# Performance work log

Measured on AMD Instinct MI355X. Metric: run time of the kernel, lower is better.

Reference implementation:

```python
import jax, jax.numpy as jnp
import numpy as np

# RReLU in eval mode acts as leaky-relu with slope (lower+upper)/2, defaults 1/8, 1/3
RRELU_SLOPE = (1.0 / 8.0 + 1.0 / 3.0) / 2.0

T, N, F, H, C, O, E = 8, 50000, 128, 128, 64, 2, 800000
HM1 = H - 1  # second GCN layer / MLP input width = hidden_feat - 1


def _glorot(k, shape):
    a = np.sqrt(6.0 / (shape[-2] + shape[-1])).astype(np.float32)
    return jax.random.uniform(k, shape, jnp.float32, -a, a)


def setup_inputs() -> dict:
    key = jax.random.key(0)
    ks = jax.random.split(key, 16)
    inp = {}
    inp["feats"] = jax.random.normal(ks[0], (T, N, F), jnp.float32)
    inp["src"] = jax.random.randint(ks[1], (E,), 0, N, jnp.int32)
    inp["dst"] = jax.random.randint(ks[2], (E,), 0, N, jnp.int32)
    # initial GCN weights (xavier_uniform as in reset_parameters)
    inp["W1_0"] = _glorot(ks[3], (F, H))
    inp["W2_0"] = _glorot(ks[4], (H, HM1))
    # mat-GRU cell 1 (rows=F, cols=H): gates stacked [z, r, h]
    inp["g1_W"] = jax.random.normal(ks[5], (3, F, F), jnp.float32) * 0.05
    inp["g1_U"] = jax.random.normal(ks[6], (3, F, F), jnp.float32) * 0.05
    inp["g1_b"] = jnp.zeros((3, F, H), jnp.float32)
    # mat-GRU cell 2 (rows=H, cols=H-1)
    inp["g2_W"] = jax.random.normal(ks[7], (3, H, H), jnp.float32) * 0.05
    inp["g2_U"] = jax.random.normal(ks[8], (3, H, H), jnp.float32) * 0.05
    inp["g2_b"] = jnp.zeros((3, H, HM1), jnp.float32)
    # MLP head
    inp["mlp_w1"] = _glorot(ks[9], (HM1, C))
    inp["mlp_b1"] = jnp.zeros((C,), jnp.float32)
    inp["mlp_w2"] = _glorot(ks[10], (C, O))
    inp["mlp_b2"] = jnp.zeros((O,), jnp.float32)
    return inp


def _mat_gru(gW, gU, gb, Wh):
    # EvolveGCN-O: weight matrix is both input and hidden of the GRU
    z = jax.nn.sigmoid(gW[0] @ Wh + gU[0] @ Wh + gb[0])
    r = jax.nn.sigmoid(gW[1] @ Wh + gU[1] @ Wh + gb[1])
    h_til = jnp.tanh(gW[2] @ Wh + gU[2] @ (r * Wh) + gb[2])
    return (1.0 - z) * Wh + z * h_til


def reference(feats, W1_0, W2_0, g1_W, g1_U, g1_b, g2_W, g2_U, g2_b,
              mlp_w1, mlp_b1, mlp_w2, mlp_b2, src, dst):
    n = feats.shape[1]
    ones = jnp.ones(src.shape, jnp.float32)
    deg_out = jax.ops.segment_sum(ones, src, num_segments=n)
    deg_in = jax.ops.segment_sum(ones, dst, num_segments=n)
    # symmetric GCN normalization D_out^-1/2 A D_in^-1/2 on edge list
    norm = (jax.lax.rsqrt(jnp.maximum(deg_out, 1.0))[src]
            * jax.lax.rsqrt(jnp.maximum(deg_in, 1.0))[dst])  # [E]

    def aggregate(x):  # x: [N, d] -> [N, d]
        return jax.ops.segment_sum(x[src] * norm[:, None], dst, num_segments=n)

    def step(carry, x):
        W1, W2, _ = carry
        W1 = _mat_gru(g1_W, g1_U, g1_b, W1)
        W2 = _mat_gru(g2_W, g2_U, g2_b, W2)
        h1 = aggregate(x @ W1)                      # [N, H]
        h1 = jnp.where(h1 >= 0, h1, RRELU_SLOPE * h1)  # RReLU (eval-mode)
        h2 = aggregate(h1 @ W2)                     # [N, H-1]
        return (W1, W2, h2), None

    feat0 = jnp.zeros((n, W2_0.shape[1]), feats.dtype)
    (W1, W2, feat_end), _ = jax.lax.scan(step, (W1_0, W2_0, feat0), feats)
    out = jnp.maximum(feat_end @ mlp_w1 + mlp_b1, 0.0) @ mlp_w2 + mlp_b2
    return out
```

## Files before the change

kernel.cpp:

```cpp
#include <hip/hip_runtime.h>


#define HM1 127

static constexpr float RRELU_SLOPE = (1.0f / 8.0f + 1.0f / 3.0f) * 0.5f;

__device__ __forceinline__ float sigmoidf_(float x) {
    return 1.0f / (1.0f + expf(-x));
}

__global__ __launch_bounds__(256) void phase1(
    const int* __restrict__ src, const int* __restrict__ dst,
    int* __restrict__ degO, int* __restrict__ degI, int E, int nbE,
    const float* __restrict__ g1W, const float* __restrict__ g1U,
    const float* __restrict__ g2W, const float* __restrict__ g2U,
    float* __restrict__ AT)
{
    int bid = blockIdx.x;
    if (bid < nbE) {
        int e = bid * 256 + threadIdx.x;
        if (e < E) {
            atomicAdd(&degO[src[e]], 1);
            atomicAdd(&degI[dst[e]], 1);
        }
    } else {
        int t = (bid - nbE) * 256 + threadIdx.x;
        int m = t >> 14;
        int k = (t >> 7) & 127;
        int i = t & 127;
        const float* W = (m < 4) ? g1W : g2W;
        const float* U = (m < 4) ? g1U : g2U;
        int which = m & 3;
        float v;
        if (which == 0)      v = W[i * 128 + k] + U[i * 128 + k];
        else if (which == 1) v = W[16384 + i * 128 + k] + U[16384 + i * 128 + k];
        else if (which == 2) v = W[32768 + i * 128 + k];
        else                 v = U[32768 + i * 128 + k];
        AT[t] = v;
    }
}

__global__ __launch_bounds__(256) void phase2(
    const float* __restrict__ W1_0, const float* __restrict__ W2_0,
    const float* __restrict__ AT,
    const float* __restrict__ g1b, const float* __restrict__ g2b,
    float* __restrict__ W1f, float* __restrict__ W2f,
    const int* __restrict__ degO, const int* __restrict__ degI,
    float* __restrict__ rdegO, float* __restrict__ rdegI,
    int* __restrict__ row_ptr, int N)
{
    __shared__ float smem[512];
    int bid = blockIdx.x;
    if (bid < 128) {
        const int half = threadIdx.x >> 7;
        const int i = threadIdx.x & 127;
        int c = bid * 2 + half;
        if (c > 254) c = 254;
        const int cell = (c >= 128) ? 1 : 0;
        const int cc = cell ? (c - 128) : c;

        const float* A  = AT + cell * 4 * 16384;
        const float* A0 = A;
        const float* A1 = A + 16384;
        const float* B0 = A + 32768;
        const float* B1 = A + 49152;
        const float* gb = cell ? g2b : g1b;
        const int   ldb = cell ? HM1 : 128;
        const float* W0 = cell ? W2_0 : W1_0;
        const int   ldw = cell ? HM1 : 128;

        float* w  = smem + half * 128;
        float* rw = smem + 256 + half * 128;

        const float zb = gb[i * ldb + cc];
        const float rb = gb[128 * ldb + i * ldb + cc];
        const float hb = gb[2 * 128 * ldb + i * ldb + cc];
        float wi = W0[i * ldw + cc];
        w[i] = wi;
        __syncthreads();

        for (int s = 0; s < 8; ++s) {
            float zacc = zb, racc = rb, tacc = hb;
            #pragma unroll 4
            for (int k = 0; k < 128; ++k) {
                float wk = w[k];
                zacc += A0[k * 128 + i] * wk;
                racc += A1[k * 128 + i] * wk;
                tacc += B0[k * 128 + i] * wk;
            }
            float r = sigmoidf_(racc);
            rw[i] = r * wi;
            __syncthreads();
            #pragma unroll 4
            for (int k = 0; k < 128; ++k)
                tacc += B1[k * 128 + i] * rw[k];
            float z = sigmoidf_(zacc);
            float t = tanhf(tacc);
            float nwi = (1.0f - z) * wi + z * t;
            __syncthreads();
            wi = nwi;
            w[i] = nwi;
            __syncthreads();
        }
        float* Wf = cell ? W2f : W1f;
        Wf[i * 128 + cc] = wi;
    } else if (bid == 128) {
        int* sums = (int*)smem;
        const int t = threadIdx.x;
        const int chunk = (N + 255) / 256;
        const int lo = t * chunk;
        const int hi = min(lo + chunk, N);
        int s = 0;
        for (int i2 = lo; i2 < hi; ++i2) s += degI[i2];
        sums[t] = s;
        __syncthreads();
        for (int off = 1; off < 256; off <<= 1) {
            int v = (t >= off) ? sums[t - off] : 0;
            __syncthreads();
            sums[t] += v;
            __syncthreads();
        }
        int base = (t > 0) ? sums[t - 1] : 0;
        for (int i2 = lo; i2 < hi; ++i2) {
            row_ptr[i2] = base;
            base += degI[i2];
        }
        if (t == 255) row_ptr[N] = sums[255];
    } else {
        int n = (bid - 129) * 256 + threadIdx.x;
        if (n < N) {
            rdegO[n] = rsqrtf(fmaxf((float)degO[n], 1.0f));
            rdegI[n] = rsqrtf(fmaxf((float)degI[n], 1.0f));
        }
    }
}

__global__ __launch_bounds__(256) void phase3(
    const int* __restrict__ src, const int* __restrict__ dst,
    const int* __restrict__ row_ptr, int* __restrict__ cursor,
    int* __restrict__ srcs, int E, int nbE,
    const float* __restrict__ x7, const float* __restrict__ W1f,
    const float* __restrict__ rdegO, float* __restrict__ Zs, int N, int nbN,
    const float* __restrict__ W2f, const float* __restrict__ mw1,
    float* __restrict__ W2m)
{
    int bid = blockIdx.x;
    if (bid < nbE) {
        int e = bid * 256 + threadIdx.x;
        if (e < E) {
            int d = dst[e];
            int pos = row_ptr[d] + atomicAdd(&cursor[d], 1);
            srcs[pos] = src[e];
        }
    } else if (bid < nbE + 2 * nbN) {
        int b = bid - nbE;
        int half = b & 1;
        int row = (b >> 1) * 256 + threadIdx.x;
        int c0 = half * 64;
        if (row >= N) return;

        float acc[64];
        #pragma unroll
        for (int j = 0; j < 64; ++j) acc[j] = 0.0f;

        const float4* xr = reinterpret_cast<const float4*>(x7 + (size_t)row * 128);
        for (int k4 = 0; k4 < 32; ++k4) {
            float4 xv = xr[k4];
            const float* wr = W1f + (k4 * 4) * 128 + c0;
            #pragma unroll
            for (int j = 0; j < 64; ++j) acc[j] += xv.x * wr[j];
            wr += 128;
            #pragma unroll
            for (int j = 0; j < 64; ++j) acc[j] += xv.y * wr[j];
            wr += 128;
            #pragma unroll
            for (int j = 0; j < 64; ++j) acc[j] += xv.z * wr[j];
            wr += 128;
            #pragma unroll
            for (int j = 0; j < 64; ++j) acc[j] += xv.w * wr[j];
        }

        float ro = rdegO[row];
        float* zr = Zs + (size_t)row * 128 + c0;
        #pragma unroll
        for (int j = 0; j < 64; j += 4) {
            float4 v;
            v.x = acc[j] * ro; v.y = acc[j + 1] * ro;
            v.z = acc[j + 2] * ro; v.w = acc[j + 3] * ro;
            *reinterpret_cast<float4*>(zr + j) = v;
        }
    } else {
        int idx = (bid - nbE - 2 * nbN) * 256 + threadIdx.x;
        int i = idx >> 6, j = idx & 63;
        float acc = 0.0f;
        for (int k = 0; k < HM1; ++k)
            acc += W2f[i * 128 + k] * mw1[k * 64 + j];
        W2m[idx] = acc;
    }
}

__global__ __launch_bounds__(256) void gather128(
    const float* __restrict__ Zs, const int* __restrict__ srcs,
    const int* __restrict__ row_ptr, const float* __restrict__ rdegI,
    float* __restrict__ H1, int N)
{
    int n = (blockIdx.x * 256 + threadIdx.x) >> 6;
    int lane = threadIdx.x & 63;
    if (n >= N) return;
    int lo = row_ptr[n], hi = row_ptr[n + 1];
    float ax = 0.0f, ay = 0.0f;
    for (int base = lo; base < hi; base += 64) {
        int cnt = min(hi - base, 64);
        int idx = (lane < cnt) ? srcs[base + lane] : 0;
        int j = 0;
        for (; j + 8 <= cnt; j += 8) {
            int s0 = __shfl(idx, j + 0), s1 = __shfl(idx, j + 1);
            int s2 = __shfl(idx, j + 2), s3 = __shfl(idx, j + 3);
            int s4 = __shfl(idx, j + 4), s5 = __shfl(idx, j + 5);
            int s6 = __shfl(idx, j + 6), s7 = __shfl(idx, j + 7);
            float2 v0 = *reinterpret_cast<const float2*>(Zs + (size_t)s0 * 128 + lane * 2);
            float2 v1 = *reinterpret_cast<const float2*>(Zs + (size_t)s1 * 128 + lane * 2);
            float2 v2 = *reinterpret_cast<const float2*>(Zs + (size_t)s2 * 128 + lane * 2);
            float2 v3 = *reinterpret_cast<const float2*>(Zs + (size_t)s3 * 128 + lane * 2);
            float2 v4 = *reinterpret_cast<const float2*>(Zs + (size_t)s4 * 128 + lane * 2);
            float2 v5 = *reinterpret_cast<const float2*>(Zs + (size_t)s5 * 128 + lane * 2);
            float2 v6 = *reinterpret_cast<const float2*>(Zs + (size_t)s6 * 128 + lane * 2);
            float2 v7 = *reinterpret_cast<const float2*>(Zs + (size_t)s7 * 128 + lane * 2);
            ax += v0.x + v1.x + v2.x + v3.x + v4.x + v5.x + v6.x + v7.x;
            ay += v0.y + v1.y + v2.y + v3.y + v4.y + v5.y + v6.y + v7.y;
        }
        for (; j < cnt; ++j) {
            int s0 = __shfl(idx, j);
            float2 v0 = *reinterpret_cast<const float2*>(Zs + (size_t)s0 * 128 + lane * 2);
            ax += v0.x;
            ay += v0.y;
        }
    }
    float ri = rdegI[n];
    ax *= ri; ay *= ri;
    ax = ax >= 0.0f ? ax : RRELU_SLOPE * ax;
    ay = ay >= 0.0f ? ay : RRELU_SLOPE * ay;
    float2 o; o.x = ax; o.y = ay;
    *reinterpret_cast<float2*>(H1 + (size_t)n * 128 + lane * 2) = o;
}

__global__ __launch_bounds__(256) void gemm_y(
    const float* __restrict__ H1, const float* __restrict__ W2m,
    const float* __restrict__ rdegO, float* __restrict__ Ys, int N)
{
    int row = blockIdx.x * 256 + threadIdx.x;
    if (row >= N) return;

    float acc[64];
    #pragma unroll
    for (int j = 0; j < 64; ++j) acc[j] = 0.0f;

    const float4* hr = reinterpret_cast<const float4*>(H1 + (size_t)row * 128);
    for (int k4 = 0; k4 < 32; ++k4) {
        float4 h = hr[k4];
        const float* wr = W2m + (k4 * 4) * 64;
        #pragma unroll
        for (int j = 0; j < 64; ++j) acc[j] += h.x * wr[j];
        wr += 64;
        #pragma unroll
        for (int j = 0; j < 64; ++j) acc[j] += h.y * wr[j];
        wr += 64;
        #pragma unroll
        for (int j = 0; j < 64; ++j) acc[j] += h.z * wr[j];
        wr += 64;
        #pragma unroll
        for (int j = 0; j < 64; ++j) acc[j] += h.w * wr[j];
    }

    float ro = rdegO[row];
    float* yr = Ys + (size_t)row * 64;
    #pragma unroll
    for (int j = 0; j < 64; j += 4) {
        float4 v;
        v.x = acc[j] * ro; v.y = acc[j + 1] * ro;
        v.z = acc[j + 2] * ro; v.w = acc[j + 3] * ro;
        *reinterpret_cast<float4*>(yr + j) = v;
    }
}

__global__ __launch_bounds__(256) void gather64_mlp(
    const float* __restrict__ Ys, const int* __restrict__ srcs,
    const int* __restrict__ row_ptr, const float* __restrict__ rdegI,
    const float* __restrict__ b1, const float* __restrict__ w2,
    const float* __restrict__ b2, float* __restrict__ out, int N)
{
    int n = (blockIdx.x * 256 + threadIdx.x) >> 6;
    int lane = threadIdx.x & 63;
    if (n >= N) return;
    int lo = row_ptr[n], hi = row_ptr[n + 1];
    float acc = 0.0f;
    for (int base = lo; base < hi; base += 64) {
        int cnt = min(hi - base, 64);
        int idx = (lane < cnt) ? srcs[base + lane] : 0;
        int j = 0;
        for (; j + 8 <= cnt; j += 8) {
            int s0 = __shfl(idx, j + 0), s1 = __shfl(idx, j + 1);
            int s2 = __shfl(idx, j + 2), s3 = __shfl(idx, j + 3);
            int s4 = __shfl(idx, j + 4), s5 = __shfl(idx, j + 5);
            int s6 = __shfl(idx, j + 6), s7 = __shfl(idx, j + 7);
            acc += Ys[(size_t)s0 * 64 + lane] + Ys[(size_t)s1 * 64 + lane]
                 + Ys[(size_t)s2 * 64 + lane] + Ys[(size_t)s3 * 64 + lane]
                 + Ys[(size_t)s4 * 64 + lane] + Ys[(size_t)s5 * 64 + lane]
                 + Ys[(size_t)s6 * 64 + lane] + Ys[(size_t)s7 * 64 + lane];
        }
        for (; j < cnt; ++j) {
            int s0 = __shfl(idx, j);
            acc += Ys[(size_t)s0 * 64 + lane];
        }
    }
    float z = acc * rdegI[n];
    float t = fmaxf(z + b1[lane], 0.0f);
    float p0 = t * w2[lane * 2 + 0];
    float p1 = t * w2[lane * 2 + 1];
    #pragma unroll
    for (int off = 32; off; off >>= 1) {
        p0 += __shfl_xor(p0, off);
        p1 += __shfl_xor(p1, off);
    }
    if (lane == 0) {
        out[(size_t)n * 2 + 0] = p0 + b2[0];
        out[(size_t)n * 2 + 1] = p1 + b2[1];
    }
}

extern "C" void kernel_launch(void* const* d_in, const int* in_sizes, int n_in,
                              void* d_out, int out_size, void* d_ws, size_t ws_size,
                              hipStream_t stream) {
    const float* feats = (const float*)d_in[0];
    const int*   src   = (const int*)d_in[1];
    const int*   dst   = (const int*)d_in[2];
    const float* W1_0  = (const float*)d_in[3];
    const float* W2_0  = (const float*)d_in[4];
    const float* g1W   = (const float*)d_in[5];
    const float* g1U   = (const float*)d_in[6];
    const float* g1b   = (const float*)d_in[7];
    const float* g2W   = (const float*)d_in[8];
    const float* g2U   = (const float*)d_in[9];
    const float* g2b   = (const float*)d_in[10];
    const float* mw1   = (const float*)d_in[11];
    const float* mb1   = (const float*)d_in[12];
    const float* mw2   = (const float*)d_in[13];
    const float* mb2   = (const float*)d_in[14];
    float* out = (float*)d_out;

    const int E = in_sizes[1];
    const int N = in_sizes[0] / (8 * 128);
    const int nbE = (E + 255) / 256;
    const int nbN = (N + 255) / 256;

    float* ws    = (float*)d_ws;
    float* W1f   = ws;
    float* W2f   = W1f + 16384;
    float* W2m   = W2f + 16384;
    float* AT    = W2m + 8192;
    float* rdegO = AT + 8 * 16384;
    float* rdegI = rdegO + N;
    int*   degO  = (int*)(rdegI + N);
    int*   degI  = degO + N;
    int*   cursor= degI + N;
    int*   row_ptr = cursor + N;
    int*   srcs  = row_ptr + N + 1;
    float* Zs    = (float*)(srcs + E);
    float* H1    = Zs + (size_t)N * 128;
    float* Ys    = Zs;

    const float* x7 = feats + (size_t)7 * N * 128;

    hipMemsetAsync(degO, 0, sizeof(int) * 3 * (size_t)N, stream);

    phase1<<<nbE + 512, 256, 0, stream>>>(src, dst, degO, degI, E, nbE,
                                          g1W, g1U, g2W, g2U, AT);

    phase2<<<129 + nbN, 256, 0, stream>>>(W1_0, W2_0, AT, g1b, g2b, W1f, W2f,
                                          degO, degI, rdegO, rdegI, row_ptr, N);

    phase3<<<nbE + 2 * nbN + 32, 256, 0, stream>>>(
        src, dst, row_ptr, cursor, srcs, E, nbE,
        x7, W1f, rdegO, Zs, N, nbN, W2f, mw1, W2m);

    int ngather = ((N * 64) + 255) / 256;
    gather128<<<ngather, 256, 0, stream>>>(Zs, srcs, row_ptr, rdegI, H1, N);

    gemm_y<<<nbN, 256, 0, stream>>>(H1, W2m, rdegO, Ys, N);

    gather64_mlp<<<ngather, 256, 0, stream>>>(Ys, srcs, row_ptr, rdegI,
                                              mb1, mw2, mb2, out, N);
}
```

Measured before the change: 635.7 us.

## Fuse gather with second GEMM, retile first GEMM, parallelize scan and transpose

Several changes land together. The gather128 and gemm_y kernels merge into one phase4 kernel that aggregates each node's row into shared memory and immediately multiplies it by W2m, so the H1 intermediate never goes through global memory. The x@W1 GEMM is retiled so each thread computes 4 rows by 16 columns with float4 weight loads, replacing one row by 64 columns per thread, which should improve weight reuse and register pressure. The single-block prefix scan now uses wave shuffles instead of serial per-thread chunks, and the GRU weight transpose moves into 32 shared-memory tiled blocks for coalesced access; in exchange the scan still runs in one block and the fused kernel adds a block barrier.

```diff
diff --git a/kernel.cpp b/kernel.cpp
--- a/kernel.cpp
+++ b/kernel.cpp
@@ -11,32 +11,49 @@
 
 __global__ __launch_bounds__(256) void phase1(
     const int* __restrict__ src, const int* __restrict__ dst,
-    int* __restrict__ degO, int* __restrict__ degI, int E, int nbE,
+    int* __restrict__ degO, int* __restrict__ degI, int E,
     const float* __restrict__ g1W, const float* __restrict__ g1U,
     const float* __restrict__ g2W, const float* __restrict__ g2U,
     float* __restrict__ AT)
 {
     int bid = blockIdx.x;
-    if (bid < nbE) {
-        int e = bid * 256 + threadIdx.x;
+    if (bid < 32) {
+        __shared__ float tile[64][65];
+        int m     = bid >> 2;
+        int itile = bid & 1;
+        int ktile = (bid >> 1) & 1;
+        const float* W = (m < 4) ? g1W : g2W;
+        const float* U = (m < 4) ? g1U : g2U;
+        int which = m & 3;
+        const float* P;
+        const float* Q2 = nullptr;
+        if (which == 0)      { P = W;         Q2 = U; }
+        else if (which == 1) { P = W + 16384; Q2 = U + 16384; }
+        else if (which == 2) { P = W + 32768; }
+        else                 { P = U + 32768; }
+        int c  = threadIdx.x & 63;
+        int r4 = threadIdx.x >> 6;
+        #pragma unroll
+        for (int rr = 0; rr < 16; ++rr) {
+            int row = itile * 64 + rr * 4 + r4;
+            int col = ktile * 64 + c;
+            float v = P[row * 128 + col];
+            if (Q2) v += Q2[row * 128 + col];
+            tile[rr * 4 + r4][c] = v;
+        }
+        __syncthreads();
+        float* ATm = AT + m * 16384;
+        #pragma unroll
+        for (int rr = 0; rr < 16; ++rr) {
+            int krow = ktile * 64 + rr * 4 + r4;
+            ATm[krow * 128 + itile * 64 + c] = tile[c][rr * 4 + r4];
+        }
+    } else {
+        int e = (bid - 32) * 256 + threadIdx.x;
         if (e < E) {
             atomicAdd(&degO[src[e]], 1);
             atomicAdd(&degI[dst[e]], 1);
         }
-    } else {
-        int t = (bid - nbE) * 256 + threadIdx.x;
-        int m = t >> 14;
-        int k = (t >> 7) & 127;
-        int i = t & 127;
-        const float* W = (m < 4) ? g1W : g2W;
-        const float* U = (m < 4) ? g1U : g2U;
-        int which = m & 3;
-        float v;
-        if (which == 0)      v = W[i * 128 + k] + U[i * 128 + k];
-        else if (which == 1) v = W[16384 + i * 128 + k] + U[16384 + i * 128 + k];
-        else if (which == 2) v = W[32768 + i * 128 + k];
-        else                 v = U[32768 + i * 128 + k];
-        AT[t] = v;
     }
 }
 
@@ -105,27 +122,33 @@
         float* Wf = cell ? W2f : W1f;
         Wf[i * 128 + cc] = wi;
     } else if (bid == 128) {
-        int* sums = (int*)smem;
-        const int t = threadIdx.x;
-        const int chunk = (N + 255) / 256;
-        const int lo = t * chunk;
-        const int hi = min(lo + chunk, N);
+        __shared__ int qsum[4];
+        const int t = threadIdx.x, w = t >> 6, l = t & 63;
+        const int Q = (((N + 3) >> 2) + 63) & ~63;
+        const int qlo = w * Q;
+        const int qhi = min(qlo + Q, N);
         int s = 0;
-        for (int i2 = lo; i2 < hi; ++i2) s += degI[i2];
-        sums[t] = s;
+        for (int i2 = qlo + l; i2 < qhi; i2 += 64) s += degI[i2];
+        #pragma unroll
+        for (int d = 32; d; d >>= 1) s += __shfl_xor(s, d);
+        if (l == 0) qsum[w] = s;
         __syncthreads();
-        for (int off = 1; off < 256; off <<= 1) {
-            int v = (t >= off) ? sums[t - off] : 0;
-            __syncthreads();
-            sums[t] += v;
-            __syncthreads();
-        }
-        int base = (t > 0) ? sums[t - 1] : 0;
-        for (int i2 = lo; i2 < hi; ++i2) {
-            row_ptr[i2] = base;
-            base += degI[i2];
-        }
-        if (t == 255) row_ptr[N] = sums[255];
+        int base = 0;
+        for (int q = 0; q < w; ++q) base += qsum[q];
+        if (t == 0) row_ptr[N] = qsum[0] + qsum[1] + qsum[2] + qsum[3];
+        int carry = base;
+        for (int b = qlo; b < qhi; b += 64) {
+            int i2 = b + l;
+            int v = (i2 < qhi) ? degI[i2] : 0;
+            int incl = v;
+            #pragma unroll
+            for (int d = 1; d < 64; d <<= 1) {
+                int nbr = __shfl_up(incl, d);
+                if (l >= d) incl += nbr;
+            }
+            if (i2 < qhi) row_ptr[i2] = carry + incl - v;
+            carry += __shfl(incl, 63);
+        }
     } else {
         int n = (bid - 129) * 256 + threadIdx.x;
         if (n < N) {
@@ -140,7 +163,7 @@
     const int* __restrict__ row_ptr, int* __restrict__ cursor,
     int* __restrict__ srcs, int E, int nbE,
     const float* __restrict__ x7, const float* __restrict__ W1f,
-    const float* __restrict__ rdegO, float* __restrict__ Zs, int N, int nbN,
+    const float* __restrict__ rdegO, float* __restrict__ Zs, int N, int ngz,
     const float* __restrict__ W2f, const float* __restrict__ mw1,
     float* __restrict__ W2m)
 {
@@ -152,45 +175,67 @@
             int pos = row_ptr[d] + atomicAdd(&cursor[d], 1);
             srcs[pos] = src[e];
         }
-    } else if (bid < nbE + 2 * nbN) {
-        int b = bid - nbE;
-        int half = b & 1;
-        int row = (b >> 1) * 256 + threadIdx.x;
-        int c0 = half * 64;
-        if (row >= N) return;
-
-        float acc[64];
+    } else if (bid < nbE + ngz) {
+        int b  = bid - nbE;
+        int cb = b & 7;
+        int rg = b >> 3;
+        int c0 = cb * 16;
+        int r0 = rg * 1024 + threadIdx.x;
+
+        float acc[4][16];
         #pragma unroll
-        for (int j = 0; j < 64; ++j) acc[j] = 0.0f;
-
-        const float4* xr = reinterpret_cast<const float4*>(x7 + (size_t)row * 128);
+        for (int r = 0; r < 4; ++r)
+            #pragma unroll
+            for (int j = 0; j < 16; ++j) acc[r][j] = 0.0f;
+
+        const float4* x0p = (const float4*)(x7 + (size_t)min(r0,       N - 1) * 128);
+        const float4* x1p = (const float4*)(x7 + (size_t)min(r0 + 256, N - 1) * 128);
+        const float4* x2p = (const float4*)(x7 + (size_t)min(r0 + 512, N - 1) * 128);
+        const float4* x3p = (const float4*)(x7 + (size_t)min(r0 + 768, N - 1) * 128);
+
         for (int k4 = 0; k4 < 32; ++k4) {
-            float4 xv = xr[k4];
-            const float* wr = W1f + (k4 * 4) * 128 + c0;
-            #pragma unroll
-            for (int j = 0; j < 64; ++j) acc[j] += xv.x * wr[j];
-            wr += 128;
-            #pragma unroll
-            for (int j = 0; j < 64; ++j) acc[j] += xv.y * wr[j];
-            wr += 128;
-            #pragma unroll
-            for (int j = 0; j < 64; ++j) acc[j] += xv.z * wr[j];
-            wr += 128;
-            #pragma unroll
-            for (int j = 0; j < 64; ++j) acc[j] += xv.w * wr[j];
-        }
-
-        float ro = rdegO[row];
-        float* zr = Zs + (size_t)row * 128 + c0;
+            float4 v0 = x0p[k4], v1 = x1p[k4], v2 = x2p[k4], v3 = x3p[k4];
+            const float* wb = W1f + (k4 * 4) * 128 + c0;
+#define ZSTEP(KK, S0, S1, S2, S3)                                           \
+            {                                                               \
+                const float* wr_ = wb + (KK) * 128;                         \
+                float4 wa = *(const float4*)(wr_ + 0);                      \
+                float4 wq = *(const float4*)(wr_ + 4);                      \
+                float4 wc = *(const float4*)(wr_ + 8);                      \
+                float4 wd = *(const float4*)(wr_ + 12);                     \
+                float w16[16] = {wa.x, wa.y, wa.z, wa.w, wq.x, wq.y, wq.z, wq.w, \
+                                 wc.x, wc.y, wc.z, wc.w, wd.x, wd.y, wd.z, wd.w}; \
+                float ss[4] = {S0, S1, S2, S3};                             \
+                _Pragma("unroll")                                           \
+                for (int r = 0; r < 4; ++r) {                               \
+                    _Pragma("unroll")                                       \
+                    for (int j = 0; j < 16; ++j) acc[r][j] += ss[r] * w16[j]; \
+                }                                                           \
+            }
+            ZSTEP(0, v0.x, v1.x, v2.x, v3.x)
+            ZSTEP(1, v0.y, v1.y, v2.y, v3.y)
+            ZSTEP(2, v0.z, v1.z, v2.z, v3.z)
+            ZSTEP(3, v0.w, v1.w, v2.w, v3.w)
+#undef ZSTEP
+        }
+
         #pragma unroll
-        for (int j = 0; j < 64; j += 4) {
-            float4 v;
-            v.x = acc[j] * ro; v.y = acc[j + 1] * ro;
-            v.z = acc[j + 2] * ro; v.w = acc[j + 3] * ro;
-            *reinterpret_cast<float4*>(zr + j) = v;
+        for (int r = 0; r < 4; ++r) {
+            int row = r0 + r * 256;
+            if (row < N) {
+                float ro = rdegO[row];
+                float* zr = Zs + (size_t)row * 128 + c0;
+                #pragma unroll
+                for (int j = 0; j < 16; j += 4) {
+                    float4 o;
+                    o.x = acc[r][j] * ro;     o.y = acc[r][j + 1] * ro;
+                    o.z = acc[r][j + 2] * ro; o.w = acc[r][j + 3] * ro;
+                    *(float4*)(zr + j) = o;
+                }
+            }
         }
     } else {
-        int idx = (bid - nbE - 2 * nbN) * 256 + threadIdx.x;
+        int idx = (bid - nbE - ngz) * 256 + threadIdx.x;
         int i = idx >> 6, j = idx & 63;
         float acc = 0.0f;
         for (int k = 0; k < HM1; ++k)
@@ -199,91 +244,63 @@
     }
 }
 
-__global__ __launch_bounds__(256) void gather128(
+__global__ __launch_bounds__(256) void phase4(
     const float* __restrict__ Zs, const int* __restrict__ srcs,
     const int* __restrict__ row_ptr, const float* __restrict__ rdegI,
-    float* __restrict__ H1, int N)
+    const float* __restrict__ rdegO, const float* __restrict__ W2m,
+    float* __restrict__ Ys, int N)
 {
-    int n = (blockIdx.x * 256 + threadIdx.x) >> 6;
-    int lane = threadIdx.x & 63;
-    if (n >= N) return;
-    int lo = row_ptr[n], hi = row_ptr[n + 1];
+    __shared__ float h[4][128];
+    const int t = threadIdx.x, w = t >> 6, l = t & 63;
+    const int n = blockIdx.x * 4 + w;
+    int lo = 0, hi = 0;
+    float ri = 0.0f;
+    if (n < N) { lo = row_ptr[n]; hi = row_ptr[n + 1]; ri = rdegI[n]; }
     float ax = 0.0f, ay = 0.0f;
     for (int base = lo; base < hi; base += 64) {
         int cnt = min(hi - base, 64);
-        int idx = (lane < cnt) ? srcs[base + lane] : 0;
+        int idx = (l < cnt) ? srcs[base + l] : 0;
         int j = 0;
         for (; j + 8 <= cnt; j += 8) {
             int s0 = __shfl(idx, j + 0), s1 = __shfl(idx, j + 1);
             int s2 = __shfl(idx, j + 2), s3 = __shfl(idx, j + 3);
             int s4 = __shfl(idx, j + 4), s5 = __shfl(idx, j + 5);
             int s6 = __shfl(idx, j + 6), s7 = __shfl(idx, j + 7);
-            float2 v0 = *reinterpret_cast<const float2*>(Zs + (size_t)s0 * 128 + lane * 2);
-            float2 v1 = *reinterpret_cast<const float2*>(Zs + (size_t)s1 * 128 + lane * 2);
-            float2 v2 = *reinterpret_cast<const float2*>(Zs + (size_t)s2 * 128 + lane * 2);
-            float2 v3 = *reinterpret_cast<const float2*>(Zs + (size_t)s3 * 128 + lane * 2);
-            float2 v4 = *reinterpret_cast<const float2*>(Zs + (size_t)s4 * 128 + lane * 2);
-            float2 v5 = *reinterpret_cast<const float2*>(Zs + (size_t)s5 * 128 + lane * 2);
-            float2 v6 = *reinterpret_cast<const float2*>(Zs + (size_t)s6 * 128 + lane * 2);
-            float2 v7 = *reinterpret_cast<const float2*>(Zs + (size_t)s7 * 128 + lane * 2);
+            float2 v0 = *(const float2*)(Zs + (size_t)s0 * 128 + l * 2);
+            float2 v1 = *(const float2*)(Zs + (size_t)s1 * 128 + l * 2);
+            float2 v2 = *(const float2*)(Zs + (size_t)s2 * 128 + l * 2);
+            float2 v3 = *(const float2*)(Zs + (size_t)s3 * 128 + l * 2);
+            float2 v4 = *(const float2*)(Zs + (size_t)s4 * 128 + l * 2);
+            float2 v5 = *(const float2*)(Zs + (size_t)s5 * 128 + l * 2);
+            float2 v6 = *(const float2*)(Zs + (size_t)s6 * 128 + l * 2);
+            float2 v7 = *(const float2*)(Zs + (size_t)s7 * 128 + l * 2);
             ax += v0.x + v1.x + v2.x + v3.x + v4.x + v5.x + v6.x + v7.x;
             ay += v0.y + v1.y + v2.y + v3.y + v4.y + v5.y + v6.y + v7.y;
         }
         for (; j < cnt; ++j) {
             int s0 = __shfl(idx, j);
-            float2 v0 = *reinterpret_cast<const float2*>(Zs + (size_t)s0 * 128 + lane * 2);
+            float2 v0 = *(const float2*)(Zs + (size_t)s0 * 128 + l * 2);
             ax += v0.x;
             ay += v0.y;
         }
     }
-    float ri = rdegI[n];
     ax *= ri; ay *= ri;
     ax = ax >= 0.0f ? ax : RRELU_SLOPE * ax;
     ay = ay >= 0.0f ? ay : RRELU_SLOPE * ay;
-    float2 o; o.x = ax; o.y = ay;
-    *reinterpret_cast<float2*>(H1 + (size_t)n * 128 + lane * 2) = o;
-}
-
-__global__ __launch_bounds__(256) void gemm_y(
-    const float* __restrict__ H1, const float* __restrict__ W2m,
-    const float* __restrict__ rdegO, float* __restrict__ Ys, int N)
-{
-    int row = blockIdx.x * 256 + threadIdx.x;
-    if (row >= N) return;
-
-    float acc[64];
-    #pragma unroll
-    for (int j = 0; j < 64; ++j) acc[j] = 0.0f;
-
-    const float4* hr = reinterpret_cast<const float4*>(H1 + (size_t)row * 128);
-    for (int k4 = 0; k4 < 32; ++k4) {
-        float4 h = hr[k4];
-        const float* wr = W2m + (k4 * 4) * 64;
-        #pragma unroll
-        for (int j = 0; j < 64; ++j) acc[j] += h.x * wr[j];
-        wr += 64;
-        #pragma unroll
-        for (int j = 0; j < 64; ++j) acc[j] += h.y * wr[j];
-        wr += 64;
-        #pragma unroll
-        for (int j = 0; j < 64; ++j) acc[j] += h.z * wr[j];
-        wr += 64;
-        #pragma unroll
-        for (int j = 0; j < 64; ++j) acc[j] += h.w * wr[j];
-    }
-
-    float ro = rdegO[row];
-    float* yr = Ys + (size_t)row * 64;
-    #pragma unroll
-    for (int j = 0; j < 64; j += 4) {
-        float4 v;
-        v.x = acc[j] * ro; v.y = acc[j + 1] * ro;
-        v.z = acc[j + 2] * ro; v.w = acc[j + 3] * ro;
-        *reinterpret_cast<float4*>(yr + j) = v;
-    }
-}
-
-__global__ __launch_bounds__(256) void gather64_mlp(
+    *(float2*)&h[w][2 * l] = make_float2(ax, ay);
+    __syncthreads();
+
+    const int n2 = blockIdx.x * 4 + w;
+    if (n2 < N) {
+        const float* hr = h[w];
+        float a = 0.0f;
+        #pragma unroll 8
+        for (int k = 0; k < 128; ++k) a += hr[k] * W2m[k * 64 + l];
+        Ys[(size_t)n2 * 64 + l] = a * rdegO[n2];
+    }
+}
+
+__global__ __launch_bounds__(256) void phase5(
     const float* __restrict__ Ys, const int* __restrict__ srcs,
     const int* __restrict__ row_ptr, const float* __restrict__ rdegI,
     const float* __restrict__ b1, const float* __restrict__ w2,
@@ -352,6 +369,7 @@
     const int N = in_sizes[0] / (8 * 128);
     const int nbE = (E + 255) / 256;
     const int nbN = (N + 255) / 256;
+    const int ngz = ((N + 1023) / 1024) * 8;
 
     float* ws    = (float*)d_ws;
     float* W1f   = ws;
@@ -366,28 +384,25 @@
     int*   row_ptr = cursor + N;
     int*   srcs  = row_ptr + N + 1;
     float* Zs    = (float*)(srcs + E);
-    float* H1    = Zs + (size_t)N * 128;
-    float* Ys    = Zs;
+    float* Ys    = Zs + (size_t)N * 128;
 
     const float* x7 = feats + (size_t)7 * N * 128;
 
     hipMemsetAsync(degO, 0, sizeof(int) * 3 * (size_t)N, stream);
 
-    phase1<<<nbE + 512, 256, 0, stream>>>(src, dst, degO, degI, E, nbE,
-                                          g1W, g1U, g2W, g2U, AT);
+    phase1<<<32 + nbE, 256, 0, stream>>>(src, dst, degO, degI, E,
+                                         g1W, g1U, g2W, g2U, AT);
 
     phase2<<<129 + nbN, 256, 0, stream>>>(W1_0, W2_0, AT, g1b, g2b, W1f, W2f,
                                           degO, degI, rdegO, rdegI, row_ptr, N);
 
-    phase3<<<nbE + 2 * nbN + 32, 256, 0, stream>>>(
+    phase3<<<nbE + ngz + 32, 256, 0, stream>>>(
         src, dst, row_ptr, cursor, srcs, E, nbE,
-        x7, W1f, rdegO, Zs, N, nbN, W2f, mw1, W2m);
-
-    int ngather = ((N * 64) + 255) / 256;
-    gather128<<<ngather, 256, 0, stream>>>(Zs, srcs, row_ptr, rdegI, H1, N);
-
-    gemm_y<<<nbN, 256, 0, stream>>>(H1, W2m, rdegO, Ys, N);
-
-    gather64_mlp<<<ngather, 256, 0, stream>>>(Ys, srcs, row_ptr, rdegI,
-                                              mb1, mw2, mb2, out, N);
-}
+        x7, W1f, rdegO, Zs, N, ngz, W2f, mw1, W2m);
+
+    phase4<<<(N + 3) / 4, 256, 0, stream>>>(Zs, srcs, row_ptr, rdegI, rdegO,
+                                            W2m, Ys, N);
+
+    phase5<<<(N + 3) / 4, 256, 0, stream>>>(Ys, srcs, row_ptr, rdegI,
+                                            mb1, mw2, mb2, out, N);
+}
```

Result: slower. 778.9 us (+22.5%).
